# Kernel optimization log

Hardware: AMD Instinct MI355X
Metric: run time of the kernel (lower is better)

Reference implementation:

```python
import jax, jax.numpy as jnp
import numpy as np

NUM_HEADS = 16

def setup_inputs() -> dict:
    key = jax.random.key(0)
    ks = jax.random.split(key, 5)
    d_model = 1024
    x = jax.random.normal(ks[0], (2, 2048, d_model), dtype=jnp.float32)
    # xavier-uniform-like scale for square [d_model, d_model] weights
    lim = float(np.sqrt(6.0 / (d_model + d_model)))
    def w(k):
        return jax.random.uniform(k, (d_model, d_model), dtype=jnp.float32, minval=-lim, maxval=lim)
    return {"x": x, "Wq": w(ks[1]), "Wk": w(ks[2]), "Wv": w(ks[3]), "Wo": w(ks[4])}

def reference(x, Wq, Wk, Wv, Wo):
    B, S, D = x.shape
    H = NUM_HEADS
    dk = D // H
    # project: torch does x @ W.T
    def split_heads(t):
        return t.reshape(B, S, H, dk).transpose(0, 2, 1, 3)  # [B,H,S,dk]
    q = split_heads(x @ Wq.T)
    k = split_heads(x @ Wk.T)
    v = split_heads(x @ Wv.T)
    scores = jnp.einsum('bhqd,bhkd->bhqk', q, k) / jnp.sqrt(jnp.float32(dk))
    causal = jnp.tril(jnp.ones((S, S), dtype=bool))  # True where attended
    scores = jnp.where(causal[None, None], scores, -jnp.inf)
    probs = jax.nn.softmax(scores, axis=-1)
    out = jnp.einsum('bhqk,bhkd->bhqd', probs, v)  # [B,H,S,dk]
    out = out.transpose(0, 2, 1, 3).reshape(B, S, D)
    return out @ Wo.T
```

## Files before the change

### kernel.cpp

```cpp
#include <hip/hip_runtime.h>
#include <stdint.h>

#define BATCH  2
#define SEQ    2048
#define DMODEL 1024
#define NHEADS 16
#define DKH    64
#define MTOT   (BATCH*SEQ)
#define VSTR   (SEQ + 32)

typedef unsigned short u16;
typedef __bf16 bf16x8 __attribute__((ext_vector_type(8)));
typedef float  f32x4  __attribute__((ext_vector_type(4)));

extern "C" __device__ float __ocml_native_exp2_f32(float);

__device__ __forceinline__ u16 f2bf(float f) {
  union { float f; uint32_t u; } v; v.f = f;
  uint32_t u = v.u;
  return (u16)((u + 0x7FFFu + ((u >> 16) & 1u)) >> 16);
}
__device__ __forceinline__ float bf2f(u16 h) {
  union { uint32_t u; float f; } v; v.u = (uint32_t)h << 16; return v.f;
}

__device__ __forceinline__ void gld_lds16(const void* g, void* l) {
  __builtin_amdgcn_global_load_lds(
      (__attribute__((address_space(1))) void*)g,
      (__attribute__((address_space(3))) void*)l, 16, 0, 0);
}

__device__ __forceinline__ uint32_t cvtpk(float lo, float hi) {
  uint32_t r;
  asm("v_cvt_pk_bf16_f32 %0, %1, %2" : "=v"(r) : "v"(lo), "v"(hi));
  return r;
}
__device__ __forceinline__ void pl16swap(uint32_t& a, uint32_t& b) {
  asm volatile("v_permlane16_swap_b32 %0, %1" : "+v"(a), "+v"(b));
}

__global__ void cvt_f32_bf16(const float* __restrict__ src, u16* __restrict__ dst) {
  size_t i = ((size_t)blockIdx.x * 256 + threadIdx.x) * 4;
  float4 f = *(const float4*)(src + i);
  ushort4 o;
  o.x = f2bf(f.x); o.y = f2bf(f.y); o.z = f2bf(f.z); o.w = f2bf(f.w);
  *(ushort4*)(dst + i) = o;
}
__global__ void cvt_w(const float* __restrict__ a, const float* __restrict__ b,
                      const float* __restrict__ c, const float* __restrict__ d,
                      u16* __restrict__ dst) {
  const float* srcs[4] = {a, b, c, d};
  const float* s = srcs[blockIdx.y];
  size_t i = ((size_t)blockIdx.x * 256 + threadIdx.x) * 4;
  float4 f = *(const float4*)(s + i);
  ushort4 o;
  o.x = f2bf(f.x); o.y = f2bf(f.y); o.z = f2bf(f.z); o.w = f2bf(f.w);
  *(ushort4*)(dst + (size_t)blockIdx.y * (DMODEL*DMODEL) + i) = o;
}

__global__ __launch_bounds__(256, 3) void gemm_qkv(
    const u16* __restrict__ xb, const u16* __restrict__ wq,
    const u16* __restrict__ wk, const u16* __restrict__ wv,
    u16* __restrict__ q, u16* __restrict__ k, u16* __restrict__ v, float qscale) {
  __shared__ __align__(16) u16 lA[128 * 64];
  __shared__ __align__(16) u16 lB[3][64 * 64];

  const int tid  = threadIdx.x;
  const int lane = tid & 63;
  const int lrow = lane & 15;
  const int quad = lane >> 4;
  const int wave = tid >> 6;
  const int wm   = (wave & 1) * 64;
  const int wn   = (wave >> 1) * 32;
  const int sx   = lrow & 7;
  const int m0 = blockIdx.x * 128, n0 = blockIdx.y * 64;
  const u16* Ws[3] = {wq, wk, wv};

  f32x4 acc[3][4][2] = {};

  for (int k0 = 0; k0 < DMODEL; k0 += 64) {
    #pragma unroll
    for (int r = 0; r < 4; ++r) {
      int off  = r * 4096 + tid * 16;
      int row  = off >> 7;
      int c16  = (off >> 4) & 7;
      int colb = (c16 ^ (row & 7)) << 4;
      gld_lds16((const char*)xb + ((size_t)(m0 + row) * DMODEL + k0) * 2 + colb,
                (char*)lA + off);
    }
    #pragma unroll
    for (int z = 0; z < 3; ++z)
      #pragma unroll
      for (int r = 0; r < 2; ++r) {
        int off  = r * 4096 + tid * 16;
        int row  = off >> 7;
        int c16  = (off >> 4) & 7;
        int colb = (c16 ^ (row & 7)) << 4;
        gld_lds16((const char*)Ws[z] + ((size_t)(n0 + row) * DMODEL + k0) * 2 + colb,
                  (char*)&lB[z][0] + off);
      }
    __syncthreads();
    #pragma unroll
    for (int ks = 0; ks < 2; ++ks) {
      const int ro = ((((ks << 2) | quad) ^ sx) << 3);
      bf16x8 a[4], b[3][2];
      #pragma unroll
      for (int i = 0; i < 4; ++i)
        a[i] = *(const bf16x8*)(lA + (wm + i*16 + lrow) * 64 + ro);
      #pragma unroll
      for (int z = 0; z < 3; ++z)
        #pragma unroll
        for (int j = 0; j < 2; ++j)
          b[z][j] = *(const bf16x8*)(&lB[z][0] + (wn + j*16 + lrow) * 64 + ro);
      #pragma unroll
      for (int z = 0; z < 3; ++z)
        #pragma unroll
        for (int i = 0; i < 4; ++i)
          #pragma unroll
          for (int j = 0; j < 2; ++j)
            acc[z][i][j] = __builtin_amdgcn_mfma_f32_16x16x32_bf16(a[i], b[z][j], acc[z][i][j], 0, 0, 0);
    }
    __syncthreads();
  }

  const int rb = quad * 4, cb = lrow;
  const int h  = blockIdx.y;
  u16* outs[3] = {q, k, v};
  #pragma unroll
  for (int z = 0; z < 3; ++z) {
    u16* out = outs[z];
    if (z == 2) {
      #pragma unroll
      for (int i = 0; i < 4; ++i)
        #pragma unroll
        for (int j = 0; j < 2; ++j) {
          int row0 = m0 + wm + i*16 + rb;
          int d_   = wn + j*16 + cb;
          int b_ = row0 >> 11, s0 = row0 & 2047;
          ushort4 pk;
          pk.x = f2bf(acc[z][i][j][0]); pk.y = f2bf(acc[z][i][j][1]);
          pk.z = f2bf(acc[z][i][j][2]); pk.w = f2bf(acc[z][i][j][3]);
          *(ushort4*)&out[((size_t)(b_*NHEADS + h) * DKH + d_) * VSTR + s0] = pk;
        }
    } else {
      const float scale = (z == 0) ? qscale : 1.0f;
      #pragma unroll
      for (int i = 0; i < 4; ++i)
        #pragma unroll
        for (int j = 0; j < 2; ++j)
          #pragma unroll
          for (int r = 0; r < 4; ++r) {
            int row = m0 + wm + i*16 + rb + r;
            int d_  = wn + j*16 + cb;
            int b_ = row >> 11, s_ = row & 2047;
            out[(((size_t)(b_*NHEADS + h) * SEQ + s_) << 6) + d_] =
                f2bf(acc[z][i][j][r] * scale);
          }
    }
  }
}

__device__ __forceinline__ void gemm_core64(const u16* A, const u16* W,
                                            int m0, int n0, f32x4 acc[4][2],
                                            u16* lA, u16* lB) {
  const int tid  = threadIdx.x;
  const int lane = tid & 63;
  const int lrow = lane & 15;
  const int quad = lane >> 4;
  const int wave = tid >> 6;
  const int wm   = (wave & 1) * 64;
  const int wn   = (wave >> 1) * 32;
  const int sx   = lrow & 7;

  for (int k0 = 0; k0 < DMODEL; k0 += 64) {
    #pragma unroll
    for (int r = 0; r < 4; ++r) {
      int off  = r * 4096 + tid * 16;
      int row  = off >> 7;
      int c16  = (off >> 4) & 7;
      int colb = (c16 ^ (row & 7)) << 4;
      gld_lds16((const char*)A + ((size_t)(m0 + row) * DMODEL + k0) * 2 + colb,
                (char*)lA + off);
    }
    #pragma unroll
    for (int r = 0; r < 2; ++r) {
      int off  = r * 4096 + tid * 16;
      int row  = off >> 7;
      int c16  = (off >> 4) & 7;
      int colb = (c16 ^ (row & 7)) << 4;
      gld_lds16((const char*)W + ((size_t)(n0 + row) * DMODEL + k0) * 2 + colb,
                (char*)lB + off);
    }
    __syncthreads();
    #pragma unroll
    for (int ks = 0; ks < 2; ++ks) {
      bf16x8 a[4], b[2];
      const int ro = ((((ks << 2) | quad) ^ sx) << 3);
      #pragma unroll
      for (int i = 0; i < 4; ++i)
        a[i] = *(const bf16x8*)(lA + (wm + i*16 + lrow) * 64 + ro);
      #pragma unroll
      for (int j = 0; j < 2; ++j)
        b[j] = *(const bf16x8*)(lB + (wn + j*16 + lrow) * 64 + ro);
      #pragma unroll
      for (int i = 0; i < 4; ++i)
        #pragma unroll
        for (int j = 0; j < 2; ++j)
          acc[i][j] = __builtin_amdgcn_mfma_f32_16x16x32_bf16(a[i], b[j], acc[i][j], 0, 0, 0);
    }
    __syncthreads();
  }
}

__global__ __launch_bounds__(256, 3) void gemm_out(
    const u16* __restrict__ ab, const u16* __restrict__ wo, float* __restrict__ out) {
  __shared__ __align__(16) u16 lA[128 * 64];
  __shared__ __align__(16) u16 lB[64 * 64];
  const int m0 = blockIdx.x * 128, n0 = blockIdx.y * 64;
  f32x4 acc[4][2] = {};
  gemm_core64(ab, wo, m0, n0, acc, lA, lB);

  const int lane = threadIdx.x & 63;
  const int wave = threadIdx.x >> 6;
  const int wm = (wave & 1) * 64, wn = (wave >> 1) * 32;
  const int rb = (lane >> 4) * 4, cb = lane & 15;
  #pragma unroll
  for (int i = 0; i < 4; ++i)
    #pragma unroll
    for (int j = 0; j < 2; ++j)
      #pragma unroll
      for (int r = 0; r < 4; ++r)
        out[(size_t)(m0 + wm + i*16 + rb + r) * DMODEL + (n0 + wn + j*16 + cb)]
            = acc[i][j][r];
}

#define PSTR 68
__device__ const uint8_t JT[80] = {
  124,125,126,127, 120,121,122, 116,117,118, 112,113,114, 108,109,110,
  104,105,106, 100,101,102, 96,97,98, 92,93,94, 88,89, 84,85, 80,81,
  76,77, 72,73, 68,69, 64,65, 60,61, 56, 52, 48, 44, 40, 36, 32, 28,
  123,90,57,24, 119,86,53,20, 115,82,49,16, 111,78,45,12,
  107,74,41,8, 103,70,37,4, 99,66,33,0
};

__global__ __launch_bounds__(64, 2) void attn(
    const u16* __restrict__ Q, const u16* __restrict__ K,
    const u16* __restrict__ V, u16* __restrict__ O,
    u16* __restrict__ po, float* __restrict__ pl) {
  const int lane = threadIdx.x & 63;
  const int lrow = lane & 15;
  const int quad = lane >> 4;
  const int kq   = quad * 8;
  const int vkq  = ((((quad & 1) << 1) | (quad >> 1)) << 3);

  const int g  = blockIdx.x >> 5;
  const int bh = blockIdx.x & 31;
  const int e  = JT[g];
  const int p  = e >> 2, c = e & 3;
  const int lo = c * 8;
  const int hi = (p + 1 < lo + 8) ? p + 1 : lo + 8;

  const u16* Qg = Q + (size_t)bh * SEQ * DKH;
  const u16* Kg = K + (size_t)bh * SEQ * DKH;
  const u16* Vg = V + (size_t)bh * DKH * VSTR;

  bf16x8 aq[4][2];
  #pragma unroll
  for (int i = 0; i < 4; ++i)
    #pragma unroll
    for (int ks = 0; ks < 2; ++ks)
      aq[i][ks] = *(const bf16x8*)(Qg + (size_t)(64*p + 16*i + lrow) * DKH + ks*32 + kq);

  f32x4 o_acc[4][4] = {};
  float l_acc[4] = {};

  const u16* kbase = Kg + (size_t)lrow * DKH + kq;
  const u16* vbase = Vg + (size_t)lrow * VSTR + vkq;

  for (int t = lo; t < hi; ++t) {
    bf16x8 kf[2][4], vf[2][4];
    #pragma unroll
    for (int ks = 0; ks < 2; ++ks)
      #pragma unroll
      for (int j = 0; j < 4; ++j) {
        kf[ks][j] = *(const bf16x8*)(kbase + (size_t)t*64*DKH + j*16*DKH + ks*32);
        vf[ks][j] = *(const bf16x8*)(vbase + t*64 + (size_t)j*16*VSTR + ks*32);
      }
    const bool mk = (t == p);

    #pragma unroll
    for (int i = 0; i < 4; ++i) {
      f32x4 s_acc[4] = {};
      #pragma unroll
      for (int ks = 0; ks < 2; ++ks)
        #pragma unroll
        for (int j = 0; j < 4; ++j)
          s_acc[j] = __builtin_amdgcn_mfma_f32_16x16x32_bf16(kf[ks][j], aq[i][ks], s_acc[j], 0, 0, 0);

      if (mk) {
        const int qloc = 16*i + lrow;
        #pragma unroll
        for (int j = 0; j < 4; ++j) {
          int kl = j*16 + quad*4;
          #pragma unroll
          for (int r = 0; r < 4; ++r)
            if (kl + r > qloc) s_acc[j][r] = -1e30f;
        }
      }

      uint32_t w[4][2];
      float ls = 0.f;
      #pragma unroll
      for (int j = 0; j < 4; ++j) {
        float p0 = __ocml_native_exp2_f32(s_acc[j][0]);
        float p1 = __ocml_native_exp2_f32(s_acc[j][1]);
        float p2 = __ocml_native_exp2_f32(s_acc[j][2]);
        float p3 = __ocml_native_exp2_f32(s_acc[j][3]);
        ls += (p0 + p1) + (p2 + p3);
        w[j][0] = cvtpk(p0, p1);
        w[j][1] = cvtpk(p2, p3);
      }
      l_acc[i] += ls;

      pl16swap(w[0][0], w[1][0]);
      pl16swap(w[0][1], w[1][1]);
      pl16swap(w[2][0], w[3][0]);
      pl16swap(w[2][1], w[3][1]);
      union { uint32_t u[4]; bf16x8 v; } g0, g1;
      g0.u[0] = w[0][0]; g0.u[1] = w[0][1]; g0.u[2] = w[1][0]; g0.u[3] = w[1][1];
      g1.u[0] = w[2][0]; g1.u[1] = w[2][1]; g1.u[2] = w[3][0]; g1.u[3] = w[3][1];

      #pragma unroll
      for (int j = 0; j < 4; ++j)
        o_acc[i][j] = __builtin_amdgcn_mfma_f32_16x16x32_bf16(g0.v, vf[0][j], o_acc[i][j], 0, 0, 0);
      #pragma unroll
      for (int j = 0; j < 4; ++j)
        o_acc[i][j] = __builtin_amdgcn_mfma_f32_16x16x32_bf16(g1.v, vf[1][j], o_acc[i][j], 0, 0, 0);
    }
  }

  float lr[4][4];
  #pragma unroll
  for (int i = 0; i < 4; ++i) {
    float s = l_acc[i];
    s += __shfl_xor(s, 16, 64);
    s += __shfl_xor(s, 32, 64);
    #pragma unroll
    for (int r = 0; r < 4; ++r)
      lr[i][r] = __shfl(s, quad*4 + r, 16);
  }

  if (p <= 7) {
    const int h = bh & 15, b_ = bh >> 4;
    #pragma unroll
    for (int i = 0; i < 4; ++i)
      #pragma unroll
      for (int j = 0; j < 4; ++j)
        #pragma unroll
        for (int r = 0; r < 4; ++r) {
          int sg = 64*p + 16*i + quad*4 + r;
          O[(size_t)(b_ * SEQ + sg) * DMODEL + h * DKH + j*16 + lrow]
              = f2bf(o_acc[i][j][r] / lr[i][r]);
        }
  } else {
    const int base = (p < 16) ? (p - 8) * 2
                   : (p < 24) ? 16 + (p - 16) * 3
                   :            40 + (p - 24) * 4;
    const int slot = (base + c) * 32 + bh;
    #pragma unroll
    for (int i = 0; i < 4; ++i) {
      #pragma unroll
      for (int j = 0; j < 4; ++j) {
        ushort4 pk;
        pk.x = f2bf(o_acc[i][j][0]); pk.y = f2bf(o_acc[i][j][1]);
        pk.z = f2bf(o_acc[i][j][2]); pk.w = f2bf(o_acc[i][j][3]);
        *(ushort4*)&po[(size_t)slot * 4096 + (j*16 + lrow) * 64 + 16*i + quad*4] = pk;
      }
      if (lrow == 0)
        #pragma unroll
        for (int r = 0; r < 4; ++r)
          pl[slot * 64 + 16*i + quad*4 + r] = lr[i][r];
    }
  }
}

__global__ __launch_bounds__(256) void combine(
    const u16* __restrict__ po, const float* __restrict__ pl, u16* __restrict__ ab) {
  __shared__ u16 Ls[64][68];
  const int b  = blockIdx.x;
  const int p  = 8 + (b >> 5);
  const int bh = b & 31;
  const int t  = threadIdx.x;
  const int col = t >> 2;
  const int r0  = (t & 3) * 16;
  const int base = (p < 16) ? (p - 8) * 2
                 : (p < 24) ? 16 + (p - 16) * 3
                 :            40 + (p - 24) * 4;
  const int nc   = (p < 16) ? 2 : (p < 24) ? 3 : 4;

  float acc[16], lsum[16];
  const size_t s0 = (size_t)(base * 32 + bh);
  const u16*   q0 = po + s0 * 4096 + col * 64 + r0;
  const float* l0 = pl + s0 * 64 + r0;
  #pragma unroll
  for (int q4 = 0; q4 < 4; ++q4) {
    ushort4 a  = *(const ushort4*)(q0 + q4 * 4);
    ushort4 c2 = *(const ushort4*)(q0 + (size_t)32 * 4096 + q4 * 4);
    acc[q4*4+0] = bf2f(a.x) + bf2f(c2.x);
    acc[q4*4+1] = bf2f(a.y) + bf2f(c2.y);
    acc[q4*4+2] = bf2f(a.z) + bf2f(c2.z);
    acc[q4*4+3] = bf2f(a.w) + bf2f(c2.w);
    float4 f = *(const float4*)(l0 + q4 * 4);
    float4 g = *(const float4*)(l0 + 32 * 64 + q4 * 4);
    lsum[q4*4+0] = f.x + g.x; lsum[q4*4+1] = f.y + g.y;
    lsum[q4*4+2] = f.z + g.z; lsum[q4*4+3] = f.w + g.w;
  }
  if (nc >= 3) {
    #pragma unroll
    for (int q4 = 0; q4 < 4; ++q4) {
      ushort4 a = *(const ushort4*)(q0 + (size_t)64 * 4096 + q4 * 4);
      acc[q4*4+0] += bf2f(a.x); acc[q4*4+1] += bf2f(a.y);
      acc[q4*4+2] += bf2f(a.z); acc[q4*4+3] += bf2f(a.w);
      float4 f = *(const float4*)(l0 + 64 * 64 + q4 * 4);
      lsum[q4*4+0] += f.x; lsum[q4*4+1] += f.y;
      lsum[q4*4+2] += f.z; lsum[q4*4+3] += f.w;
    }
  }
  if (nc == 4) {
    #pragma unroll
    for (int q4 = 0; q4 < 4; ++q4) {
      ushort4 a = *(const ushort4*)(q0 + (size_t)96 * 4096 + q4 * 4);
      acc[q4*4+0] += bf2f(a.x); acc[q4*4+1] += bf2f(a.y);
      acc[q4*4+2] += bf2f(a.z); acc[q4*4+3] += bf2f(a.w);
      float4 f = *(const float4*)(l0 + 96 * 64 + q4 * 4);
      lsum[q4*4+0] += f.x; lsum[q4*4+1] += f.y;
      lsum[q4*4+2] += f.z; lsum[q4*4+3] += f.w;
    }
  }
  #pragma unroll
  for (int q = 0; q < 16; ++q)
    Ls[r0 + q][col] = f2bf(acc[q] / lsum[q]);
  __syncthreads();

  const int row = t >> 2;
  const int c0  = (t & 3) * 16;
  const int b_ = bh >> 4, h = bh & 15;
  u16* dst = ab + (size_t)(b_ * SEQ + 64 * p + row) * DMODEL + h * DKH + c0;
  #pragma unroll
  for (int q = 0; q < 16; q += 4)
    *(ushort4*)(dst + q) = *(const ushort4*)&Ls[row][c0 + q];
}

extern "C" void kernel_launch(void* const* d_in, const int* in_sizes, int n_in,
                              void* d_out, int out_size, void* d_ws, size_t ws_size,
                              hipStream_t stream) {
  const float* x  = (const float*)d_in[0];
  const float* Wq = (const float*)d_in[1];
  const float* Wk = (const float*)d_in[2];
  const float* Wv = (const float*)d_in[3];
  const float* Wo = (const float*)d_in[4];
  float* out = (float*)d_out;

  u16* xb  = (u16*)d_ws;
  u16* wqb = xb  + (size_t)MTOT * DMODEL;
  u16* wkb = wqb + (size_t)DMODEL * DMODEL;
  u16* wvb = wkb + (size_t)DMODEL * DMODEL;
  u16* wob = wvb + (size_t)DMODEL * DMODEL;
  u16* qb  = wob + (size_t)DMODEL * DMODEL;
  u16* kb  = qb  + (size_t)MTOT * DMODEL;
  u16* vb  = kb  + (size_t)MTOT * DMODEL;
  u16* ab  = vb  + (size_t)BATCH * NHEADS * DKH * VSTR;
  u16* po  = ab  + (size_t)MTOT * DMODEL;
  float* pl = (float*)(po + (size_t)2304 * 4096);

  cvt_f32_bf16<<<MTOT * DMODEL / 1024, 256, 0, stream>>>(x, xb);
  cvt_w<<<dim3(DMODEL * DMODEL / 1024, 4), 256, 0, stream>>>(Wq, Wk, Wv, Wo, wqb);

  const float qscale = 0.125f * 1.44269504088896340736f;
  gemm_qkv<<<dim3(32, 16), 256, 0, stream>>>(
      xb, wqb, wkb, wvb, qb, kb, vb, qscale);

  attn<<<2560, 64, 0, stream>>>(qb, kb, vb, ab, po, pl);
  combine<<<768, 256, 0, stream>>>(po, pl, ab);

  gemm_out<<<dim3(32, 16), 256, 0, stream>>>(ab, wob, out);
}
```

Measured before the change: 169.1 us.

## Split attention query rows across four waves sharing double-buffered LDS K/V tiles

The attention kernel now launches 256 threads per block instead of one wave. Each wave handles 16 query rows instead of 64. K/V tiles are staged into XOR-swizzled, double-buffered shared memory with direct global-to-LDS loads, and the next tile is prefetched while the current one is computed. This replaces per-wave redundant global K/V fragment loads with one shared copy and spreads work over more waves. It adds a block barrier per tile and uses 32KB of LDS per block.

Result: no change. 167.2 us (-1.1%).

```diff
diff --git a/kernel.cpp b/kernel.cpp
--- a/kernel.cpp
+++ b/kernel.cpp
@@ -234,7 +234,6 @@
             = acc[i][j][r];
 }
 
-#define PSTR 68
 __device__ const uint8_t JT[80] = {
   124,125,126,127, 120,121,122, 116,117,118, 112,113,114, 108,109,110,
   104,105,106, 100,101,102, 96,97,98, 92,93,94, 88,89, 84,85, 80,81,
@@ -243,15 +242,34 @@
   107,74,41,8, 103,70,37,4, 99,66,33,0
 };
 
-__global__ __launch_bounds__(64, 2) void attn(
+__device__ __forceinline__ void stage_kv(const u16* Kg, const u16* Vg, int t,
+                                         u16* lK, u16* lV, int tid) {
+  #pragma unroll
+  for (int r = 0; r < 2; ++r) {
+    int off  = r * 4096 + tid * 16;
+    int row  = off >> 7;
+    int colb = (((off >> 4) & 7) ^ (row & 7)) << 4;
+    gld_lds16((const char*)Kg + ((size_t)(t*64 + row) * DKH) * 2 + colb,
+              (char*)lK + off);
+    gld_lds16((const char*)Vg + ((size_t)row * VSTR + t*64) * 2 + colb,
+              (char*)lV + off);
+  }
+}
+
+__global__ __launch_bounds__(256, 4) void attn(
     const u16* __restrict__ Q, const u16* __restrict__ K,
     const u16* __restrict__ V, u16* __restrict__ O,
     u16* __restrict__ po, float* __restrict__ pl) {
-  const int lane = threadIdx.x & 63;
+  __shared__ __align__(16) u16 lK[2][64 * 64];
+  __shared__ __align__(16) u16 lV[2][64 * 64];
+
+  const int tid  = threadIdx.x;
+  const int wid  = tid >> 6;
+  const int lane = tid & 63;
   const int lrow = lane & 15;
   const int quad = lane >> 4;
-  const int kq   = quad * 8;
-  const int vkq  = ((((quad & 1) << 1) | (quad >> 1)) << 3);
+  const int sx   = lrow & 7;
+  const int pq   = ((quad & 1) << 1) | (quad >> 1);
 
   const int g  = blockIdx.x >> 5;
   const int bh = blockIdx.x & 31;
@@ -264,123 +282,121 @@
   const u16* Kg = K + (size_t)bh * SEQ * DKH;
   const u16* Vg = V + (size_t)bh * DKH * VSTR;
 
-  bf16x8 aq[4][2];
-  #pragma unroll
-  for (int i = 0; i < 4; ++i)
+  bf16x8 aq[2];
+  #pragma unroll
+  for (int ks = 0; ks < 2; ++ks)
+    aq[ks] = *(const bf16x8*)(Qg + (size_t)(64*p + 16*wid + lrow) * DKH + ks*32 + quad*8);
+
+  f32x4 o_acc[4] = {};
+  float l_acc = 0.f;
+
+  stage_kv(Kg, Vg, lo, &lK[0][0], &lV[0][0], tid);
+  __syncthreads();
+  int cur = 0;
+
+  for (int t = lo; t < hi; ++t) {
+    if (t + 1 < hi)
+      stage_kv(Kg, Vg, t + 1, &lK[cur ^ 1][0], &lV[cur ^ 1][0], tid);
+
+    bf16x8 kf[2][4], vf[2][4];
+    #pragma unroll
+    for (int ks = 0; ks < 2; ++ks) {
+      const int kro = ((((ks << 2) | quad) ^ sx) << 3);
+      const int vro = ((((ks << 2) | pq)   ^ sx) << 3);
+      #pragma unroll
+      for (int j = 0; j < 4; ++j) {
+        kf[ks][j] = *(const bf16x8*)(&lK[cur][0] + (j*16 + lrow) * 64 + kro);
+        vf[ks][j] = *(const bf16x8*)(&lV[cur][0] + (j*16 + lrow) * 64 + vro);
+      }
+    }
+
+    f32x4 s_acc[4] = {};
     #pragma unroll
     for (int ks = 0; ks < 2; ++ks)
-      aq[i][ks] = *(const bf16x8*)(Qg + (size_t)(64*p + 16*i + lrow) * DKH + ks*32 + kq);
-
-  f32x4 o_acc[4][4] = {};
-  float l_acc[4] = {};
-
-  const u16* kbase = Kg + (size_t)lrow * DKH + kq;
-  const u16* vbase = Vg + (size_t)lrow * VSTR + vkq;
-
-  for (int t = lo; t < hi; ++t) {
-    bf16x8 kf[2][4], vf[2][4];
-    #pragma unroll
-    for (int ks = 0; ks < 2; ++ks)
+      #pragma unroll
+      for (int j = 0; j < 4; ++j)
+        s_acc[j] = __builtin_amdgcn_mfma_f32_16x16x32_bf16(kf[ks][j], aq[ks], s_acc[j], 0, 0, 0);
+
+    if (t == p) {
+      const int qloc = 16*wid + lrow;
       #pragma unroll
       for (int j = 0; j < 4; ++j) {
-        kf[ks][j] = *(const bf16x8*)(kbase + (size_t)t*64*DKH + j*16*DKH + ks*32);
-        vf[ks][j] = *(const bf16x8*)(vbase + t*64 + (size_t)j*16*VSTR + ks*32);
+        int kl = j*16 + quad*4;
+        #pragma unroll
+        for (int r = 0; r < 4; ++r)
+          if (kl + r > qloc) s_acc[j][r] = -1e30f;
       }
-    const bool mk = (t == p);
-
-    #pragma unroll
-    for (int i = 0; i < 4; ++i) {
-      f32x4 s_acc[4] = {};
-      #pragma unroll
-      for (int ks = 0; ks < 2; ++ks)
-        #pragma unroll
-        for (int j = 0; j < 4; ++j)
-          s_acc[j] = __builtin_amdgcn_mfma_f32_16x16x32_bf16(kf[ks][j], aq[i][ks], s_acc[j], 0, 0, 0);
-
-      if (mk) {
-        const int qloc = 16*i + lrow;
-        #pragma unroll
-        for (int j = 0; j < 4; ++j) {
-          int kl = j*16 + quad*4;
-          #pragma unroll
-          for (int r = 0; r < 4; ++r)
-            if (kl + r > qloc) s_acc[j][r] = -1e30f;
-        }
-      }
-
-      uint32_t w[4][2];
-      float ls = 0.f;
-      #pragma unroll
-      for (int j = 0; j < 4; ++j) {
-        float p0 = __ocml_native_exp2_f32(s_acc[j][0]);
-        float p1 = __ocml_native_exp2_f32(s_acc[j][1]);
-        float p2 = __ocml_native_exp2_f32(s_acc[j][2]);
-        float p3 = __ocml_native_exp2_f32(s_acc[j][3]);
-        ls += (p0 + p1) + (p2 + p3);
-        w[j][0] = cvtpk(p0, p1);
-        w[j][1] = cvtpk(p2, p3);
-      }
-      l_acc[i] += ls;
-
-      pl16swap(w[0][0], w[1][0]);
-      pl16swap(w[0][1], w[1][1]);
-      pl16swap(w[2][0], w[3][0]);
-      pl16swap(w[2][1], w[3][1]);
-      union { uint32_t u[4]; bf16x8 v; } g0, g1;
-      g0.u[0] = w[0][0]; g0.u[1] = w[0][1]; g0.u[2] = w[1][0]; g0.u[3] = w[1][1];
-      g1.u[0] = w[2][0]; g1.u[1] = w[2][1]; g1.u[2] = w[3][0]; g1.u[3] = w[3][1];
-
-      #pragma unroll
-      for (int j = 0; j < 4; ++j)
-        o_acc[i][j] = __builtin_amdgcn_mfma_f32_16x16x32_bf16(g0.v, vf[0][j], o_acc[i][j], 0, 0, 0);
-      #pragma unroll
-      for (int j = 0; j < 4; ++j)
-        o_acc[i][j] = __builtin_amdgcn_mfma_f32_16x16x32_bf16(g1.v, vf[1][j], o_acc[i][j], 0, 0, 0);
-    }
-  }
-
-  float lr[4][4];
-  #pragma unroll
-  for (int i = 0; i < 4; ++i) {
-    float s = l_acc[i];
+    }
+
+    uint32_t w[4][2];
+    float ls = 0.f;
+    #pragma unroll
+    for (int j = 0; j < 4; ++j) {
+      float p0 = __ocml_native_exp2_f32(s_acc[j][0]);
+      float p1 = __ocml_native_exp2_f32(s_acc[j][1]);
+      float p2 = __ocml_native_exp2_f32(s_acc[j][2]);
+      float p3 = __ocml_native_exp2_f32(s_acc[j][3]);
+      ls += (p0 + p1) + (p2 + p3);
+      w[j][0] = cvtpk(p0, p1);
+      w[j][1] = cvtpk(p2, p3);
+    }
+    l_acc += ls;
+
+    pl16swap(w[0][0], w[1][0]);
+    pl16swap(w[0][1], w[1][1]);
+    pl16swap(w[2][0], w[3][0]);
+    pl16swap(w[2][1], w[3][1]);
+    union { uint32_t u[4]; bf16x8 v; } g0, g1;
+    g0.u[0] = w[0][0]; g0.u[1] = w[0][1]; g0.u[2] = w[1][0]; g0.u[3] = w[1][1];
+    g1.u[0] = w[2][0]; g1.u[1] = w[2][1]; g1.u[2] = w[3][0]; g1.u[3] = w[3][1];
+
+    #pragma unroll
+    for (int j = 0; j < 4; ++j)
+      o_acc[j] = __builtin_amdgcn_mfma_f32_16x16x32_bf16(g0.v, vf[0][j], o_acc[j], 0, 0, 0);
+    #pragma unroll
+    for (int j = 0; j < 4; ++j)
+      o_acc[j] = __builtin_amdgcn_mfma_f32_16x16x32_bf16(g1.v, vf[1][j], o_acc[j], 0, 0, 0);
+
+    __syncthreads();
+    cur ^= 1;
+  }
+
+  float lr[4];
+  {
+    float s = l_acc;
     s += __shfl_xor(s, 16, 64);
     s += __shfl_xor(s, 32, 64);
     #pragma unroll
     for (int r = 0; r < 4; ++r)
-      lr[i][r] = __shfl(s, quad*4 + r, 16);
+      lr[r] = __shfl(s, quad*4 + r, 16);
   }
 
   if (p <= 7) {
     const int h = bh & 15, b_ = bh >> 4;
     #pragma unroll
-    for (int i = 0; i < 4; ++i)
-      #pragma unroll
-      for (int j = 0; j < 4; ++j)
-        #pragma unroll
-        for (int r = 0; r < 4; ++r) {
-          int sg = 64*p + 16*i + quad*4 + r;
-          O[(size_t)(b_ * SEQ + sg) * DMODEL + h * DKH + j*16 + lrow]
-              = f2bf(o_acc[i][j][r] / lr[i][r]);
-        }
+    for (int j = 0; j < 4; ++j)
+      #pragma unroll
+      for (int r = 0; r < 4; ++r) {
+        int sg = 64*p + 16*wid + quad*4 + r;
+        O[(size_t)(b_ * SEQ + sg) * DMODEL + h * DKH + j*16 + lrow]
+            = f2bf(o_acc[j][r] / lr[r]);
+      }
   } else {
     const int base = (p < 16) ? (p - 8) * 2
                    : (p < 24) ? 16 + (p - 16) * 3
                    :            40 + (p - 24) * 4;
     const int slot = (base + c) * 32 + bh;
     #pragma unroll
-    for (int i = 0; i < 4; ++i) {
-      #pragma unroll
-      for (int j = 0; j < 4; ++j) {
-        ushort4 pk;
-        pk.x = f2bf(o_acc[i][j][0]); pk.y = f2bf(o_acc[i][j][1]);
-        pk.z = f2bf(o_acc[i][j][2]); pk.w = f2bf(o_acc[i][j][3]);
-        *(ushort4*)&po[(size_t)slot * 4096 + (j*16 + lrow) * 64 + 16*i + quad*4] = pk;
-      }
-      if (lrow == 0)
-        #pragma unroll
-        for (int r = 0; r < 4; ++r)
-          pl[slot * 64 + 16*i + quad*4 + r] = lr[i][r];
-    }
+    for (int j = 0; j < 4; ++j) {
+      ushort4 pk;
+      pk.x = f2bf(o_acc[j][0]); pk.y = f2bf(o_acc[j][1]);
+      pk.z = f2bf(o_acc[j][2]); pk.w = f2bf(o_acc[j][3]);
+      *(ushort4*)&po[(size_t)slot * 4096 + (j*16 + lrow) * 64 + 16*wid + quad*4] = pk;
+    }
+    if (lrow == 0)
+      #pragma unroll
+      for (int r = 0; r < 4; ++r)
+        pl[slot * 64 + 16*wid + quad*4 + r] = lr[r];
   }
 }
 
@@ -480,7 +496,7 @@
   gemm_qkv<<<dim3(32, 16), 256, 0, stream>>>(
       xb, wqb, wkb, wvb, qb, kb, vb, qscale);
 
-  attn<<<2560, 64, 0, stream>>>(qb, kb, vb, ab, po, pl);
+  attn<<<2560, 256, 0, stream>>>(qb, kb, vb, ab, po, pl);
   combine<<<768, 256, 0, stream>>>(po, pl, ab);
 
   gemm_out<<<dim3(32, 16), 256, 0, stream>>>(ab, wob, out);
```
